# Performance work log

Measured on AMD Instinct MI355X. Metric: run time of the kernel, lower is better.

## Reference

```python
import jax, jax.numpy as jnp
import numpy as np

B, N, DIM = 2, 2048, 512
H, DH = 8, 64
INNER = H * DH
SCALE = DH ** -0.5


def setup_inputs() -> dict:
    key = jax.random.key(0)
    ks = jax.random.split(key, 8)
    s = 0.02
    return {
        "nodes": jax.random.normal(ks[0], (B, N, DIM), dtype=jnp.float32),
        "edge_mask": jax.random.bernoulli(ks[1], 0.9, (B, N, N)),
        "wq": jax.random.normal(ks[2], (DIM, INNER), dtype=jnp.float32) * s,
        "bq": jnp.zeros((INNER,), dtype=jnp.float32),
        "wkv": jax.random.normal(ks[3], (DIM, 2 * INNER), dtype=jnp.float32) * s,
        "bkv": jnp.zeros((2 * INNER,), dtype=jnp.float32),
        "wo": jax.random.normal(ks[4], (INNER, DIM), dtype=jnp.float32) * s,
        "bo": jnp.zeros((DIM,), dtype=jnp.float32),
    }


def reference(nodes, edge_mask, wq, bq, wkv, bkv, wo, bo):
    b, n, _ = nodes.shape
    q = nodes @ wq + bq                      # [b, n, h*dh]
    kv = nodes @ wkv + bkv                   # [b, n, 2*h*dh]
    k, v = jnp.split(kv, 2, axis=-1)
    # split heads -> [b, h, n, dh]
    split = lambda t: t.reshape(b, n, H, DH).transpose(0, 2, 1, 3)
    q, k, v = split(q), split(k), split(v)
    sim = jnp.einsum('bhid,bhjd->bhij', q, k) * SCALE
    max_neg = -jnp.finfo(sim.dtype).max
    sim = jnp.where(edge_mask[:, None, :, :], sim, max_neg)
    attn = jax.nn.softmax(sim, axis=-1)
    out = jnp.einsum('bhij,bhjd->bhid', attn, v)      # [b, h, n, dh]
    out = out.transpose(0, 2, 1, 3).reshape(b, n, INNER)
    return out @ wo + bo
```

## Files before the change

kernel.cpp:

```cpp
#include <hip/hip_runtime.h>
#include <cstdint>
#include <cstddef>

#define DEVI __device__ __forceinline__

typedef __bf16 bf16x8 __attribute__((ext_vector_type(8)));
typedef float floatx4 __attribute__((ext_vector_type(4)));
typedef unsigned short us4v __attribute__((ext_vector_type(4)));
typedef unsigned short us8 __attribute__((ext_vector_type(8)));

static_assert(sizeof(bf16x8) == 16, "bf16x8 must be 16B");
static_assert(sizeof(us8) == 16, "us8 must be 16B");


#if __has_builtin(__builtin_amdgcn_cvt_pk_bf16_f32)
DEVI unsigned short f2bf(float f) {
  typedef __bf16 bf16x2 __attribute__((ext_vector_type(2)));
  union { bf16x2 v; unsigned short u[2]; } c;
  c.v = __builtin_amdgcn_cvt_pk_bf16_f32(f, 0.f);
  return c.u[0];
}
#else
DEVI unsigned short f2bf(float f) {
  unsigned int u = __float_as_uint(f);
  u += 0x7fffu + ((u >> 16) & 1u);
  return (unsigned short)(u >> 16);
}
#endif

DEVI float exp2c(float x) {
#if __has_builtin(__builtin_amdgcn_exp2f)
  return __builtin_amdgcn_exp2f(x);
#else
  return exp2f(x);
#endif
}

DEVI bf16x8 ld8(const unsigned short* p) { return *(const bf16x8*)p; }

typedef const __attribute__((address_space(1))) void* gas_ptr;
typedef __attribute__((address_space(3))) void* las_ptr;

DEVI void gld16(const void* g, void* l) {
  __builtin_amdgcn_global_load_lds((gas_ptr)g, (las_ptr)l, 16, 0, 0);
}

#define WAIT_LGKM0() __builtin_amdgcn_s_waitcnt(0xc07f)


__global__ void detect_k(const unsigned int* m, int* flag) {
  __shared__ int bad;
  if (threadIdx.x == 0) bad = 0;
  __syncthreads();
  int loc = 0;
  for (int i = threadIdx.x; i < 4096; i += 256) {
    unsigned int v = m[i];
    if (v > 1u && v != 0x3f800000u) loc = 1;
  }
  if (loc) atomicOr(&bad, 1);
  __syncthreads();
  if (threadIdx.x == 0) *flag = bad;
}

__global__ __launch_bounds__(256) void pack_k(const void* m, const int* flag,
                                              unsigned int* pm) {
  int t = blockIdx.x * 256 + threadIdx.x;
  int lane = threadIdx.x & 63;
  int byteMode = *flag;
  unsigned int n;
  if (byteMode) {
    unsigned int x = ((const unsigned int*)m)[t];
    n = ((x & 0xffu) ? 1u : 0u) | ((x & 0xff00u) ? 2u : 0u) |
        ((x & 0xff0000u) ? 4u : 0u) | ((x >> 24) ? 8u : 0u);
  } else {
    uint4 v = ((const uint4*)m)[t];
    n = (v.x ? 1u : 0u) | (v.y ? 2u : 0u) | (v.z ? 4u : 0u) | (v.w ? 8u : 0u);
  }
  unsigned int w = n << ((lane & 7) * 4);
  w |= __shfl_xor(w, 1);
  w |= __shfl_xor(w, 2);
  w |= __shfl_xor(w, 4);
  if ((lane & 7) == 0) pm[t >> 3] = w;
}

__global__ void cvt_x_k(const float* __restrict__ x, unsigned short* __restrict__ xb) {
  int i = blockIdx.x * 256 + threadIdx.x;
  float4 v = ((const float4*)x)[i];
  us4v o;
  o[0] = f2bf(v.x); o[1] = f2bf(v.y); o[2] = f2bf(v.z); o[3] = f2bf(v.w);
  *(us4v*)(xb + (size_t)i * 4) = o;
}

__global__ __launch_bounds__(256) void transpose_w_k(const float* __restrict__ src,
                                                     unsigned short* __restrict__ dst,
                                                     int C, int c0) {
  __shared__ unsigned short t2[64 * 64];
  const int t = threadIdx.x;
  const int ct = blockIdx.x * 64, rt = blockIdx.y * 64;
  for (int p = 0; p < 4; p++) {
    int kl = p * 16 + (t >> 4);
    int cc = (t & 15) * 4;
    float4 v = *(const float4*)&src[(size_t)(rt + kl) * C + ct + cc];
    float f[4] = {v.x, v.y, v.z, v.w};
    for (int i = 0; i < 4; i++) {
      int c = cc + i;
      t2[c * 64 + (kl ^ (c & 56))] = f2bf(f[i]);
    }
  }
  __syncthreads();
  for (int p = 0; p < 2; p++) {
    int c = p * 32 + (t >> 3);
    int kc = (t & 7) * 8;
    us8 v = *(const us8*)&t2[c * 64 + (kc ^ (c & 56))];
    *(us8*)&dst[(size_t)(c0 + ct + c) * 512 + rt + kc] = v;
  }
}

__global__ __launch_bounds__(256) void transpose_v_k(const unsigned short* __restrict__ v,
                                                     unsigned short* __restrict__ vt) {
  __shared__ unsigned short t2[64 * 64];
  const int t = threadIdx.x;
  const int bh = blockIdx.y;
  const int nt = blockIdx.x * 64;
  const unsigned short* src = v + (size_t)bh * 2048 * 64;
  unsigned short* dst = vt + (size_t)bh * 64 * 2048;
  for (int p = 0; p < 2; p++) {
    int nl = p * 32 + (t >> 3);
    int dc = (t & 7) * 8;
    us8 in = *(const us8*)&src[(size_t)(nt + nl) * 64 + dc];
    for (int i = 0; i < 8; i++) {
      int d = dc + i;
      t2[d * 64 + (nl ^ (d & 56))] = in[i];
    }
  }
  __syncthreads();
  for (int p = 0; p < 2; p++) {
    int d = p * 32 + (t >> 3);
    int nc = (t & 7) * 8;
    us8 o = *(const us8*)&t2[d * 64 + (nc ^ (d & 56))];
    *(us8*)&dst[(size_t)d * 2048 + nt + nc] = o;
  }
}

__global__ __launch_bounds__(256) void gemm_qkv_k(
    const unsigned short* __restrict__ A,
    const unsigned short* __restrict__ Bt,
    const float* __restrict__ bq, const float* __restrict__ bkv,
    unsigned short* __restrict__ Qo, unsigned short* __restrict__ Ko,
    unsigned short* __restrict__ Vo) {
  __shared__ unsigned short smem[8192];
  unsigned short* sA = smem;
  unsigned short* sB = smem + 4096;
  const int tid = threadIdx.x;
  const int wave = tid >> 6, lane = tid & 63, quad = lane >> 4, l16 = lane & 15;
  const int wm = wave >> 1, wn = wave & 1;
  const int bm = blockIdx.x, bn = blockIdx.y;
  floatx4 acc[4][4] = {};
  const int srow = tid >> 2;
  const int sg = (tid & 3) ^ (srow & 3);
  for (int kt = 0; kt < 16; kt++) {
    __syncthreads();
    for (int p = 0; p < 2; p++) {
      int row = p * 64 + srow;
      int g = (tid & 3) ^ (row & 3);
      gld16(&A [(size_t)(bm * 128 + row) * 512 + kt * 32 + g * 8],
            &sA[(p * 256 + wave * 64) * 8]);
      gld16(&Bt[(size_t)(bn * 128 + row) * 512 + kt * 32 + g * 8],
            &sB[(p * 256 + wave * 64) * 8]);
    }
    __syncthreads();
    bf16x8 aF[4], bF[4];
    int swz = (quad ^ (l16 & 3)) * 8;
    for (int i = 0; i < 4; i++) aF[i] = ld8(&sA[(wm * 64 + i * 16 + l16) * 32 + swz]);
    for (int j = 0; j < 4; j++) bF[j] = ld8(&sB[(wn * 64 + j * 16 + l16) * 32 + swz]);
    for (int i = 0; i < 4; i++)
      for (int j = 0; j < 4; j++)
        acc[i][j] = __builtin_amdgcn_mfma_f32_16x16x32_bf16(aF[i], bF[j], acc[i][j], 0, 0, 0);
  }

  const int sec = bn * 2 + wn;
  float bias[4];
  float scale = 1.0f;
  if (sec < 8) {
    for (int j = 0; j < 4; j++) bias[j] = bq[sec * 64 + j * 16 + l16];
    scale = 0.18033688011112042f;
  } else {
    for (int j = 0; j < 4; j++) bias[j] = bkv[(sec - 8) * 64 + j * 16 + l16];
  }
  unsigned short* reg = smem + wave * 2048;
  for (int h = 0; h < 2; h++) {
    __syncthreads();
    for (int i2 = 0; i2 < 2; i2++) {
      int i = h * 2 + i2;
      for (int j = 0; j < 4; j++) {
        int csw = ((j ^ quad) * 16) + l16;
        for (int r = 0; r < 4; r++) {
          int rloc = i2 * 16 + quad * 4 + r;
          reg[rloc * 64 + csw] = f2bf((acc[i][j][r] + bias[j]) * scale);
        }
      }
    }
    __syncthreads();
    for (int p = 0; p < 4; p++) {
      int rloc = p * 8 + (lane >> 3);
      int c8 = lane & 7;
      int qr = (rloc >> 2) & 3;
      us8 v = *(const us8*)(reg + rloc * 64 + ((c8 * 8) ^ (qr * 16)));
      int gr = bm * 128 + wm * 64 + h * 32 + rloc;
      int n = gr & 2047, b = gr >> 11, d0 = c8 * 8;
      unsigned short* dst;
      if (sec < 8)       dst = Qo + ((size_t)(b * 8 + sec)      * 2048 + n) * 64 + d0;
      else if (sec < 16) dst = Ko + ((size_t)(b * 8 + sec - 8)  * 2048 + n) * 64 + d0;
      else               dst = Vo + ((size_t)(b * 8 + sec - 16) * 2048 + n) * 64 + d0;
      *(us8*)dst = v;
    }
  }
  (void)sg;
}

__global__ __launch_bounds__(256) void attn_k(
    const unsigned short* __restrict__ Q,
    const unsigned short* __restrict__ K,
    const unsigned short* __restrict__ Vt,
    const unsigned int* __restrict__ pm,
    unsigned short* __restrict__ AO) {
  __shared__ unsigned short kT[2][4096];
  __shared__ unsigned short vT[2][4096];
  __shared__ unsigned short pA[4][1024];
  const int tid = threadIdx.x;
  const int wave = tid >> 6, lane = tid & 63, quad = lane >> 4, l16 = lane & 15;
  const int qt = blockIdx.x, bh = blockIdx.y, b = bh >> 3, h = bh & 7;
  const int q0 = qt * 64 + wave * 16;
  const unsigned short* Qb = Q + (size_t)bh * 2048 * 64;
  const unsigned short* Kb = K + (size_t)bh * 2048 * 64;
  const unsigned short* Vb = Vt + (size_t)bh * 64 * 2048;
  const unsigned int* pmB = pm + (size_t)b * 2048 * 64;

  bf16x8 qF[2];
  qF[0] = ld8(&Qb[(size_t)(q0 + l16) * 64 + quad * 8]);
  qF[1] = ld8(&Qb[(size_t)(q0 + l16) * 64 + 32 + quad * 8]);

  floatx4 oacc[4] = {};
  float lrow[4] = {0.f, 0.f, 0.f, 0.f};

  const int srow = tid >> 3;
  const int sc = tid & 7;
  auto stageKV = [&](int tile, int buf) {
    const int k0 = tile * 64;
    for (int p = 0; p < 2; p++) {
      int row = p * 32 + srow;
      int g = sc ^ (row & 7);
      gld16(&Kb[(size_t)(k0 + row) * 64 + g * 8], &kT[buf][(p * 256 + wave * 64) * 8]);
      gld16(&Vb[(size_t)row * 2048 + k0 + g * 8], &vT[buf][(p * 256 + wave * 64) * 8]);
    }
  };

  stageKV(0, 0);
  const int sw0 = (quad ^ (l16 & 7)) * 8;
  const int sw1 = ((4 + quad) ^ (l16 & 7)) * 8;

  for (int it = 0; it < 32; ++it) {
    const int cur = it & 1;
    __syncthreads();
    if (it + 1 < 32) stageKV(it + 1, cur ^ 1);

    const unsigned short* kc = kT[cur];
    const unsigned short* vc = vT[cur];

    uint2 mw[4];
    for (int r = 0; r < 4; r++)
      mw[r] = *(const uint2*)&pmB[(size_t)(q0 + quad * 4 + r) * 64 + it * 2];

    floatx4 sim[4];
    for (int cb = 0; cb < 4; cb++) {
      bf16x8 kf0 = ld8(&kc[(cb * 16 + l16) * 64 + sw0]);
      bf16x8 kf1 = ld8(&kc[(cb * 16 + l16) * 64 + sw1]);
      floatx4 z = {0.f, 0.f, 0.f, 0.f};
      z = __builtin_amdgcn_mfma_f32_16x16x32_bf16(qF[0], kf0, z, 0, 0, 0);
      sim[cb] = __builtin_amdgcn_mfma_f32_16x16x32_bf16(qF[1], kf1, z, 0, 0, 0);
    }

    float pv[4][4];
    for (int r = 0; r < 4; r++) {
      unsigned int s0 = mw[r].x >> l16;
      unsigned int s1 = mw[r].y >> l16;
      float p0 = exp2c(sim[0][r]) * (float)(s0 & 1u);
      float p1 = exp2c(sim[1][r]) * (float)((s0 >> 16) & 1u);
      float p2 = exp2c(sim[2][r]) * (float)(s1 & 1u);
      float p3 = exp2c(sim[3][r]) * (float)((s1 >> 16) & 1u);
      lrow[r] += (p0 + p1) + (p2 + p3);
      pv[0][r] = p0; pv[1][r] = p1; pv[2][r] = p2; pv[3][r] = p3;
    }

    unsigned short* pw = pA[wave];
    const int ci = l16 & 7;
    for (int cb = 0; cb < 4; cb++) {
      int cg = cb * 2 + (l16 >> 3);
      for (int r = 0; r < 4; r++) {
        int row = quad * 4 + r;
        pw[row * 64 + ((cg ^ (row & 7)) * 8) + ci] = f2bf(pv[cb][r]);
      }
    }
    WAIT_LGKM0();
    bf16x8 pF0 = ld8(&pw[l16 * 64 + sw0]);
    bf16x8 pF1 = ld8(&pw[l16 * 64 + sw1]);
    for (int nb = 0; nb < 4; nb++) {
      bf16x8 vf0 = ld8(&vc[(nb * 16 + l16) * 64 + sw0]);
      bf16x8 vf1 = ld8(&vc[(nb * 16 + l16) * 64 + sw1]);
      oacc[nb] = __builtin_amdgcn_mfma_f32_16x16x32_bf16(pF0, vf0, oacc[nb], 0, 0, 0);
      oacc[nb] = __builtin_amdgcn_mfma_f32_16x16x32_bf16(pF1, vf1, oacc[nb], 0, 0, 0);
    }
  }

  for (int r = 0; r < 4; r++) {
    float s = lrow[r];
    s += __shfl_xor(s, 1, 16);
    s += __shfl_xor(s, 2, 16);
    s += __shfl_xor(s, 4, 16);
    s += __shfl_xor(s, 8, 16);
    lrow[r] = 1.0f / s;
  }

  unsigned short* pw = pA[wave];
  const int ci = l16 & 7;
  for (int nb = 0; nb < 4; nb++) {
    int cg = nb * 2 + (l16 >> 3);
    for (int r = 0; r < 4; r++) {
      int row = quad * 4 + r;
      pw[row * 64 + ((cg ^ (row & 7)) * 8) + ci] = f2bf(oacc[nb][r] * lrow[r]);
    }
  }
  WAIT_LGKM0();
  for (int p = 0; p < 2; p++) {
    int row = p * 8 + (lane >> 3);
    int c8 = lane & 7;
    us8 v = *(const us8*)&pw[row * 64 + ((c8 ^ (row & 7)) * 8)];
    *(us8*)&AO[((size_t)b * 2048 + q0 + row) * 512 + h * 64 + c8 * 8] = v;
  }
}

__global__ __launch_bounds__(256) void gemm_out_k(
    const unsigned short* __restrict__ A,
    const unsigned short* __restrict__ Bt,
    const float* __restrict__ bo, float* __restrict__ out) {
  __shared__ unsigned short sA[128 * 32];
  __shared__ unsigned short sB[128 * 32];
  const int tid = threadIdx.x;
  const int wave = tid >> 6, lane = tid & 63, quad = lane >> 4, l16 = lane & 15;
  const int wm = wave >> 1, wn = wave & 1;
  const int bm = blockIdx.x, bn = blockIdx.y;
  floatx4 acc[4][4] = {};
  const int srow = tid >> 2;
  for (int kt = 0; kt < 16; kt++) {
    __syncthreads();
    for (int p = 0; p < 2; p++) {
      int row = p * 64 + srow;
      int g = (tid & 3) ^ (row & 3);
      gld16(&A [(size_t)(bm * 128 + row) * 512 + kt * 32 + g * 8],
            &sA[(p * 256 + wave * 64) * 8]);
      gld16(&Bt[(size_t)(bn * 128 + row) * 512 + kt * 32 + g * 8],
            &sB[(p * 256 + wave * 64) * 8]);
    }
    __syncthreads();
    bf16x8 aF[4], bF[4];
    int swz = (quad ^ (l16 & 3)) * 8;
    for (int i = 0; i < 4; i++) aF[i] = ld8(&sA[(wm * 64 + i * 16 + l16) * 32 + swz]);
    for (int j = 0; j < 4; j++) bF[j] = ld8(&sB[(wn * 64 + j * 16 + l16) * 32 + swz]);
    for (int i = 0; i < 4; i++)
      for (int j = 0; j < 4; j++)
        acc[i][j] = __builtin_amdgcn_mfma_f32_16x16x32_bf16(aF[i], bF[j], acc[i][j], 0, 0, 0);
  }
  for (int i = 0; i < 4; i++) {
    for (int j = 0; j < 4; j++) {
      int gc = bn * 128 + wn * 64 + j * 16 + l16;
      for (int r = 0; r < 4; r++) {
        int gr = bm * 128 + wm * 64 + i * 16 + quad * 4 + r;
        out[(size_t)gr * 512 + gc] = acc[i][j][r] + bo[gc];
      }
    }
  }
}

extern "C" void kernel_launch(void* const* d_in, const int* in_sizes, int n_in,
                              void* d_out, int out_size, void* d_ws, size_t ws_size,
                              hipStream_t stream) {
  const float* nodes = (const float*)d_in[0];
  const void*  mask  = d_in[1];
  const float* wq    = (const float*)d_in[2];
  const float* bq    = (const float*)d_in[3];
  const float* wkv   = (const float*)d_in[4];
  const float* bkv   = (const float*)d_in[5];
  const float* wo    = (const float*)d_in[6];
  const float* bo    = (const float*)d_in[7];
  float* out = (float*)d_out;

  char* ws = (char*)d_ws;
  unsigned short* XB    = (unsigned short*)(ws + 0);
  unsigned short* WQKVT = (unsigned short*)(ws + 4194304);
  unsigned short* WOT   = (unsigned short*)(ws + 5767168);
  unsigned short* Qm    = (unsigned short*)(ws + 6291456);
  unsigned short* Km    = (unsigned short*)(ws + 10485760);
  unsigned short* Vm    = (unsigned short*)(ws + 14680064);
  unsigned short* VTm   = (unsigned short*)(ws + 18874368);
  unsigned short* AOm   = (unsigned short*)(ws + 23068672);
  unsigned int*   PM    = (unsigned int*)(ws + 27262976);
  int*            FLAG  = (int*)(ws + 28311552);

  detect_k<<<1, 256, 0, stream>>>((const unsigned int*)mask, FLAG);
  pack_k<<<8192, 256, 0, stream>>>(mask, FLAG, PM);
  cvt_x_k<<<2048, 256, 0, stream>>>(nodes, XB);
  transpose_w_k<<<dim3(8, 8),  256, 0, stream>>>(wq,  WQKVT, 512, 0);
  transpose_w_k<<<dim3(16, 8), 256, 0, stream>>>(wkv, WQKVT, 1024, 512);
  transpose_w_k<<<dim3(8, 8),  256, 0, stream>>>(wo,  WOT, 512, 0);
  gemm_qkv_k<<<dim3(32, 12), 256, 0, stream>>>(XB, WQKVT, bq, bkv, Qm, Km, Vm);
  transpose_v_k<<<dim3(32, 16), 256, 0, stream>>>(Vm, VTm);
  attn_k<<<dim3(32, 16), 256, 0, stream>>>(Qm, Km, VTm, PM, AOm);
  gemm_out_k<<<dim3(32, 4), 256, 0, stream>>>(AOm, WOT, bo, out);
}
```

Baseline: 184.8 us.

## Fuse launches, write V transposed from QKV GEMM, restructure attention kernel

```diff
diff --git a/kernel.cpp b/kernel.cpp
--- a/kernel.cpp
+++ b/kernel.cpp
@@ -8,6 +8,7 @@
 typedef float floatx4 __attribute__((ext_vector_type(4)));
 typedef unsigned short us4v __attribute__((ext_vector_type(4)));
 typedef unsigned short us8 __attribute__((ext_vector_type(8)));
+typedef short short4v __attribute__((ext_vector_type(4)));
 
 static_assert(sizeof(bf16x8) == 16, "bf16x8 must be 16B");
 static_assert(sizeof(us8) == 16, "us8 must be 16B");
@@ -47,29 +48,22 @@
 
 #define WAIT_LGKM0() __builtin_amdgcn_s_waitcnt(0xc07f)
 
-
-__global__ void detect_k(const unsigned int* m, int* flag) {
-  __shared__ int bad;
-  if (threadIdx.x == 0) bad = 0;
+__global__ __launch_bounds__(256) void pack_k(const void* m, unsigned int* pm) {
+  __shared__ int mode;
+  const unsigned int* md = (const unsigned int*)m;
+  unsigned int probe = md[threadIdx.x];
+  bool odd = (probe > 1u && probe != 0x3f800000u);
+  if (threadIdx.x == 0) mode = 0;
   __syncthreads();
-  int loc = 0;
-  for (int i = threadIdx.x; i < 4096; i += 256) {
-    unsigned int v = m[i];
-    if (v > 1u && v != 0x3f800000u) loc = 1;
-  }
-  if (loc) atomicOr(&bad, 1);
+  if (odd) atomicOr(&mode, 1);
   __syncthreads();
-  if (threadIdx.x == 0) *flag = bad;
-}
-
-__global__ __launch_bounds__(256) void pack_k(const void* m, const int* flag,
-                                              unsigned int* pm) {
+  int byteMode = mode;
+
   int t = blockIdx.x * 256 + threadIdx.x;
   int lane = threadIdx.x & 63;
-  int byteMode = *flag;
   unsigned int n;
   if (byteMode) {
-    unsigned int x = ((const unsigned int*)m)[t];
+    unsigned int x = md[t];
     n = ((x & 0xffu) ? 1u : 0u) | ((x & 0xff00u) ? 2u : 0u) |
         ((x & 0xff0000u) ? 4u : 0u) | ((x >> 24) ? 8u : 0u);
   } else {
@@ -91,9 +85,15 @@
   *(us4v*)(xb + (size_t)i * 4) = o;
 }
 
-__global__ __launch_bounds__(256) void transpose_w_k(const float* __restrict__ src,
-                                                     unsigned short* __restrict__ dst,
-                                                     int C, int c0) {
+__global__ __launch_bounds__(256) void transpose_all_k(
+    const float* __restrict__ wq, const float* __restrict__ wkv,
+    const float* __restrict__ wo,
+    unsigned short* __restrict__ WQKVT, unsigned short* __restrict__ WOT) {
+  const float* src; unsigned short* dst; int C, c0;
+  int z = blockIdx.z;
+  if (z == 0)      { if (blockIdx.x >= 8) return; src = wq;  dst = WQKVT; C = 512;  c0 = 0; }
+  else if (z == 1) { src = wkv; dst = WQKVT; C = 1024; c0 = 512; }
+  else             { if (blockIdx.x >= 8) return; src = wo;  dst = WOT;  C = 512;  c0 = 0; }
   __shared__ unsigned short t2[64 * 64];
   const int t = threadIdx.x;
   const int ct = blockIdx.x * 64, rt = blockIdx.y * 64;
@@ -116,64 +116,41 @@
   }
 }
 
-__global__ __launch_bounds__(256) void transpose_v_k(const unsigned short* __restrict__ v,
-                                                     unsigned short* __restrict__ vt) {
-  __shared__ unsigned short t2[64 * 64];
-  const int t = threadIdx.x;
-  const int bh = blockIdx.y;
-  const int nt = blockIdx.x * 64;
-  const unsigned short* src = v + (size_t)bh * 2048 * 64;
-  unsigned short* dst = vt + (size_t)bh * 64 * 2048;
-  for (int p = 0; p < 2; p++) {
-    int nl = p * 32 + (t >> 3);
-    int dc = (t & 7) * 8;
-    us8 in = *(const us8*)&src[(size_t)(nt + nl) * 64 + dc];
-    for (int i = 0; i < 8; i++) {
-      int d = dc + i;
-      t2[d * 64 + (nl ^ (d & 56))] = in[i];
-    }
-  }
-  __syncthreads();
-  for (int p = 0; p < 2; p++) {
-    int d = p * 32 + (t >> 3);
-    int nc = (t & 7) * 8;
-    us8 o = *(const us8*)&t2[d * 64 + (nc ^ (d & 56))];
-    *(us8*)&dst[(size_t)d * 2048 + nt + nc] = o;
-  }
-}
-
 __global__ __launch_bounds__(256) void gemm_qkv_k(
     const unsigned short* __restrict__ A,
     const unsigned short* __restrict__ Bt,
     const float* __restrict__ bq, const float* __restrict__ bkv,
     unsigned short* __restrict__ Qo, unsigned short* __restrict__ Ko,
-    unsigned short* __restrict__ Vo) {
+    unsigned short* __restrict__ VTo) {
   __shared__ unsigned short smem[8192];
   unsigned short* sA = smem;
-  unsigned short* sB = smem + 4096;
+  unsigned short* sB = smem + 2048;
   const int tid = threadIdx.x;
   const int wave = tid >> 6, lane = tid & 63, quad = lane >> 4, l16 = lane & 15;
   const int wm = wave >> 1, wn = wave & 1;
   const int bm = blockIdx.x, bn = blockIdx.y;
-  floatx4 acc[4][4] = {};
-  const int srow = tid >> 2;
-  const int sg = (tid & 3) ^ (srow & 3);
+  floatx4 acc[2][4] = {};
+  const int arow = lane >> 2;
+  const int ag = lane & 3;
   for (int kt = 0; kt < 16; kt++) {
     __syncthreads();
-    for (int p = 0; p < 2; p++) {
-      int row = p * 64 + srow;
-      int g = (tid & 3) ^ (row & 3);
-      gld16(&A [(size_t)(bm * 128 + row) * 512 + kt * 32 + g * 8],
-            &sA[(p * 256 + wave * 64) * 8]);
-      gld16(&Bt[(size_t)(bn * 128 + row) * 512 + kt * 32 + g * 8],
-            &sB[(p * 256 + wave * 64) * 8]);
-    }
-    __syncthreads();
-    bf16x8 aF[4], bF[4];
+    {
+      int rowA = wave * 16 + arow;
+      int gA = ag ^ (rowA & 3);
+      gld16(&A[(size_t)(bm * 64 + rowA) * 512 + kt * 32 + gA * 8], &sA[(wave * 16) * 32]);
+      for (int p = 0; p < 2; p++) {
+        int rowB = p * 64 + wave * 16 + arow;
+        int gB = ag ^ (rowB & 3);
+        gld16(&Bt[(size_t)(bn * 128 + rowB) * 512 + kt * 32 + gB * 8],
+              &sB[(p * 64 + wave * 16) * 32]);
+      }
+    }
+    __syncthreads();
+    bf16x8 aF[2], bF[4];
     int swz = (quad ^ (l16 & 3)) * 8;
-    for (int i = 0; i < 4; i++) aF[i] = ld8(&sA[(wm * 64 + i * 16 + l16) * 32 + swz]);
+    for (int i = 0; i < 2; i++) aF[i] = ld8(&sA[(wm * 32 + i * 16 + l16) * 32 + swz]);
     for (int j = 0; j < 4; j++) bF[j] = ld8(&sB[(wn * 64 + j * 16 + l16) * 32 + swz]);
-    for (int i = 0; i < 4; i++)
+    for (int i = 0; i < 2; i++)
       for (int j = 0; j < 4; j++)
         acc[i][j] = __builtin_amdgcn_mfma_f32_16x16x32_bf16(aF[i], bF[j], acc[i][j], 0, 0, 0);
   }
@@ -187,147 +164,142 @@
   } else {
     for (int j = 0; j < 4; j++) bias[j] = bkv[(sec - 8) * 64 + j * 16 + l16];
   }
-  unsigned short* reg = smem + wave * 2048;
-  for (int h = 0; h < 2; h++) {
-    __syncthreads();
-    for (int i2 = 0; i2 < 2; i2++) {
-      int i = h * 2 + i2;
+  const int gr0 = bm * 64 + wm * 32;
+  const int b = gr0 >> 11, n0 = gr0 & 2047;
+  unsigned short* pw = smem + wave * 2048;
+  __syncthreads();
+  if (sec < 16) {
+    for (int i = 0; i < 2; i++)
       for (int j = 0; j < 4; j++) {
-        int csw = ((j ^ quad) * 16) + l16;
+        int cg = j * 2 + (l16 >> 3), ci = l16 & 7;
         for (int r = 0; r < 4; r++) {
-          int rloc = i2 * 16 + quad * 4 + r;
-          reg[rloc * 64 + csw] = f2bf((acc[i][j][r] + bias[j]) * scale);
+          int row = i * 16 + quad * 4 + r;
+          pw[row * 64 + ((cg ^ (row & 7)) * 8) + ci] = f2bf((acc[i][j][r] + bias[j]) * scale);
         }
       }
-    }
-    __syncthreads();
+    WAIT_LGKM0();
+    unsigned short* dst = (sec < 8) ? Qo + ((size_t)(b * 8 + sec) * 2048 + n0) * 64
+                                    : Ko + ((size_t)(b * 8 + sec - 8) * 2048 + n0) * 64;
     for (int p = 0; p < 4; p++) {
-      int rloc = p * 8 + (lane >> 3);
+      int row = p * 8 + (lane >> 3);
       int c8 = lane & 7;
-      int qr = (rloc >> 2) & 3;
-      us8 v = *(const us8*)(reg + rloc * 64 + ((c8 * 8) ^ (qr * 16)));
-      int gr = bm * 128 + wm * 64 + h * 32 + rloc;
-      int n = gr & 2047, b = gr >> 11, d0 = c8 * 8;
-      unsigned short* dst;
-      if (sec < 8)       dst = Qo + ((size_t)(b * 8 + sec)      * 2048 + n) * 64 + d0;
-      else if (sec < 16) dst = Ko + ((size_t)(b * 8 + sec - 8)  * 2048 + n) * 64 + d0;
-      else               dst = Vo + ((size_t)(b * 8 + sec - 16) * 2048 + n) * 64 + d0;
-      *(us8*)dst = v;
-    }
-  }
-  (void)sg;
-}
-
-__global__ __launch_bounds__(256) void attn_k(
+      us8 v = *(const us8*)&pw[row * 64 + ((c8 ^ (row & 7)) * 8)];
+      *(us8*)&dst[(size_t)row * 64 + c8 * 8] = v;
+    }
+  } else {
+    for (int i = 0; i < 2; i++)
+      for (int j = 0; j < 4; j++) {
+        int d = j * 16 + l16;
+        int ng = i * 2 + (quad >> 1), n7 = (quad & 1) * 4;
+        for (int r = 0; r < 4; r++)
+          pw[d * 32 + ((ng ^ (d & 3)) * 8) + n7 + r] = f2bf(acc[i][j][r] + bias[j]);
+      }
+    WAIT_LGKM0();
+    unsigned short* dst = VTo + (size_t)(b * 8 + sec - 16) * 64 * 2048 + n0;
+    for (int p = 0; p < 4; p++) {
+      int d = p * 16 + (lane >> 2);
+      int c4 = lane & 3;
+      us8 v = *(const us8*)&pw[d * 32 + ((c4 ^ (d & 3)) * 8)];
+      *(us8*)&dst[(size_t)d * 2048 + c4 * 8] = v;
+    }
+  }
+}
+
+__global__ __launch_bounds__(128, 4) void attn_k(
     const unsigned short* __restrict__ Q,
     const unsigned short* __restrict__ K,
     const unsigned short* __restrict__ Vt,
     const unsigned int* __restrict__ pm,
     unsigned short* __restrict__ AO) {
-  __shared__ unsigned short kT[2][4096];
-  __shared__ unsigned short vT[2][4096];
-  __shared__ unsigned short pA[4][1024];
+  __shared__ unsigned short kT[4096];
+  __shared__ unsigned short vT[4096];
+  __shared__ unsigned short pA[2][1024];
   const int tid = threadIdx.x;
   const int wave = tid >> 6, lane = tid & 63, quad = lane >> 4, l16 = lane & 15;
   const int qt = blockIdx.x, bh = blockIdx.y, b = bh >> 3, h = bh & 7;
-  const int q0 = qt * 64 + wave * 16;
+  const int q0 = qt * 32 + wave * 16;
   const unsigned short* Qb = Q + (size_t)bh * 2048 * 64;
   const unsigned short* Kb = K + (size_t)bh * 2048 * 64;
   const unsigned short* Vb = Vt + (size_t)bh * 64 * 2048;
   const unsigned int* pmB = pm + (size_t)b * 2048 * 64;
 
-  bf16x8 qF[2];
-  qF[0] = ld8(&Qb[(size_t)(q0 + l16) * 64 + quad * 8]);
-  qF[1] = ld8(&Qb[(size_t)(q0 + l16) * 64 + 32 + quad * 8]);
+  bf16x8 qF0 = ld8(&Qb[(size_t)(q0 + l16) * 64 + quad * 8]);
+  bf16x8 qF1 = ld8(&Qb[(size_t)(q0 + l16) * 64 + 32 + quad * 8]);
 
   floatx4 oacc[4] = {};
-  float lrow[4] = {0.f, 0.f, 0.f, 0.f};
-
-  const int srow = tid >> 3;
-  const int sc = tid & 7;
-  auto stageKV = [&](int tile, int buf) {
-    const int k0 = tile * 64;
-    for (int p = 0; p < 2; p++) {
-      int row = p * 32 + srow;
-      int g = sc ^ (row & 7);
-      gld16(&Kb[(size_t)(k0 + row) * 64 + g * 8], &kT[buf][(p * 256 + wave * 64) * 8]);
-      gld16(&Vb[(size_t)row * 2048 + k0 + g * 8], &vT[buf][(p * 256 + wave * 64) * 8]);
-    }
-  };
-
-  stageKV(0, 0);
+  float lsum = 0.f;
+
   const int sw0 = (quad ^ (l16 & 7)) * 8;
   const int sw1 = ((4 + quad) ^ (l16 & 7)) * 8;
+  const int srow = wave * 8 + (lane >> 3);
+  const int sg = lane & 7;
+  const int vg = ((quad >> 1) ^ (l16 & 7)) * 8;
 
   for (int it = 0; it < 32; ++it) {
-    const int cur = it & 1;
-    __syncthreads();
-    if (it + 1 < 32) stageKV(it + 1, cur ^ 1);
-
-    const unsigned short* kc = kT[cur];
-    const unsigned short* vc = vT[cur];
-
-    uint2 mw[4];
-    for (int r = 0; r < 4; r++)
-      mw[r] = *(const uint2*)&pmB[(size_t)(q0 + quad * 4 + r) * 64 + it * 2];
-
-    floatx4 sim[4];
-    for (int cb = 0; cb < 4; cb++) {
-      bf16x8 kf0 = ld8(&kc[(cb * 16 + l16) * 64 + sw0]);
-      bf16x8 kf1 = ld8(&kc[(cb * 16 + l16) * 64 + sw1]);
+    const int k0 = it * 64;
+    __syncthreads();
+    for (int p = 0; p < 4; p++) {
+      int row = p * 16 + srow;
+      int g = sg ^ (row & 7);
+      gld16(&Kb[(size_t)(k0 + row) * 64 + g * 8], &kT[(p * 16 + wave * 8) * 64]);
+      gld16(&Vb[(size_t)row * 2048 + k0 + g * 8], &vT[(p * 16 + wave * 8) * 64]);
+    }
+    uint2 mw = *(const uint2*)&pmB[(size_t)(q0 + l16) * 64 + it * 2];
+    __syncthreads();
+
+    floatx4 st[4];
+    for (int kb = 0; kb < 4; kb++) {
+      bf16x8 kf0 = ld8(&kT[(kb * 16 + l16) * 64 + sw0]);
+      bf16x8 kf1 = ld8(&kT[(kb * 16 + l16) * 64 + sw1]);
       floatx4 z = {0.f, 0.f, 0.f, 0.f};
-      z = __builtin_amdgcn_mfma_f32_16x16x32_bf16(qF[0], kf0, z, 0, 0, 0);
-      sim[cb] = __builtin_amdgcn_mfma_f32_16x16x32_bf16(qF[1], kf1, z, 0, 0, 0);
-    }
-
-    float pv[4][4];
+      z = __builtin_amdgcn_mfma_f32_16x16x32_bf16(kf0, qF0, z, 0, 0, 0);
+      st[kb] = __builtin_amdgcn_mfma_f32_16x16x32_bf16(kf1, qF1, z, 0, 0, 0);
+    }
+
+    union { short4v s4; unsigned short u[4]; unsigned int d[2]; } pf[4];
+    for (int kb = 0; kb < 4; kb++) {
+      unsigned int w = (kb < 2) ? mw.x : mw.y;
+      int base = (kb & 1) * 16 + quad * 4;
+      for (int r = 0; r < 4; r++) {
+        float e = exp2c(st[kb][r]);
+        e = ((w >> (base + r)) & 1u) ? e : 0.f;
+        lsum += e;
+        pf[kb].u[r] = f2bf(e);
+      }
+    }
+
+#if __has_builtin(__builtin_amdgcn_mfma_f32_16x16x16bf16_1k)
+    for (int kb = 0; kb < 4; kb++) {
+      int off = ((kb * 2 + (quad >> 1)) ^ (l16 & 7)) * 8 + (quad & 1) * 4;
+      for (int db = 0; db < 4; db++) {
+        short4v a = *(const short4v*)&vT[(db * 16 + l16) * 64 + off];
+        oacc[db] = __builtin_amdgcn_mfma_f32_16x16x16bf16_1k(a, pf[kb].s4, oacc[db], 0, 0, 0);
+      }
+    }
+#else
+    for (int kb = 0; kb < 4; kb++) {
+      union { bf16x8 v; unsigned int d[4]; } bf;
+      if (quad & 1) { bf.d[0] = 0; bf.d[1] = 0; bf.d[2] = pf[kb].d[0]; bf.d[3] = pf[kb].d[1]; }
+      else          { bf.d[0] = pf[kb].d[0]; bf.d[1] = pf[kb].d[1]; bf.d[2] = 0; bf.d[3] = 0; }
+      int off = ((kb * 2 + (quad >> 1)) ^ (l16 & 7)) * 8;
+      for (int db = 0; db < 4; db++) {
+        bf16x8 a = ld8(&vT[(db * 16 + l16) * 64 + off]);
+        oacc[db] = __builtin_amdgcn_mfma_f32_16x16x32_bf16(a, bf.v, oacc[db], 0, 0, 0);
+      }
+    }
+#endif
+  }
+
+  lsum += __shfl_xor(lsum, 16);
+  lsum += __shfl_xor(lsum, 32);
+  float inv = 1.0f / lsum;
+
+  unsigned short* pw = pA[wave];
+  for (int db = 0; db < 4; db++) {
+    int cg = db * 2 + (quad >> 1);
     for (int r = 0; r < 4; r++) {
-      unsigned int s0 = mw[r].x >> l16;
-      unsigned int s1 = mw[r].y >> l16;
-      float p0 = exp2c(sim[0][r]) * (float)(s0 & 1u);
-      float p1 = exp2c(sim[1][r]) * (float)((s0 >> 16) & 1u);
-      float p2 = exp2c(sim[2][r]) * (float)(s1 & 1u);
-      float p3 = exp2c(sim[3][r]) * (float)((s1 >> 16) & 1u);
-      lrow[r] += (p0 + p1) + (p2 + p3);
-      pv[0][r] = p0; pv[1][r] = p1; pv[2][r] = p2; pv[3][r] = p3;
-    }
-
-    unsigned short* pw = pA[wave];
-    const int ci = l16 & 7;
-    for (int cb = 0; cb < 4; cb++) {
-      int cg = cb * 2 + (l16 >> 3);
-      for (int r = 0; r < 4; r++) {
-        int row = quad * 4 + r;
-        pw[row * 64 + ((cg ^ (row & 7)) * 8) + ci] = f2bf(pv[cb][r]);
-      }
-    }
-    WAIT_LGKM0();
-    bf16x8 pF0 = ld8(&pw[l16 * 64 + sw0]);
-    bf16x8 pF1 = ld8(&pw[l16 * 64 + sw1]);
-    for (int nb = 0; nb < 4; nb++) {
-      bf16x8 vf0 = ld8(&vc[(nb * 16 + l16) * 64 + sw0]);
-      bf16x8 vf1 = ld8(&vc[(nb * 16 + l16) * 64 + sw1]);
-      oacc[nb] = __builtin_amdgcn_mfma_f32_16x16x32_bf16(pF0, vf0, oacc[nb], 0, 0, 0);
-      oacc[nb] = __builtin_amdgcn_mfma_f32_16x16x32_bf16(pF1, vf1, oacc[nb], 0, 0, 0);
-    }
-  }
-
-  for (int r = 0; r < 4; r++) {
-    float s = lrow[r];
-    s += __shfl_xor(s, 1, 16);
-    s += __shfl_xor(s, 2, 16);
-    s += __shfl_xor(s, 4, 16);
-    s += __shfl_xor(s, 8, 16);
-    lrow[r] = 1.0f / s;
-  }
-
-  unsigned short* pw = pA[wave];
-  const int ci = l16 & 7;
-  for (int nb = 0; nb < 4; nb++) {
-    int cg = nb * 2 + (l16 >> 3);
-    for (int r = 0; r < 4; r++) {
-      int row = quad * 4 + r;
-      pw[row * 64 + ((cg ^ (row & 7)) * 8) + ci] = f2bf(oacc[nb][r] * lrow[r]);
+      int col = db * 16 + quad * 4 + r;
+      pw[l16 * 64 + ((cg ^ (l16 & 7)) * 8) + (col & 7)] = f2bf(oacc[db][r] * inv);
     }
   }
   WAIT_LGKM0();
@@ -337,48 +309,54 @@
     us8 v = *(const us8*)&pw[row * 64 + ((c8 ^ (row & 7)) * 8)];
     *(us8*)&AO[((size_t)b * 2048 + q0 + row) * 512 + h * 64 + c8 * 8] = v;
   }
+  (void)vg;
 }
 
 __global__ __launch_bounds__(256) void gemm_out_k(
     const unsigned short* __restrict__ A,
     const unsigned short* __restrict__ Bt,
     const float* __restrict__ bo, float* __restrict__ out) {
-  __shared__ unsigned short sA[128 * 32];
-  __shared__ unsigned short sB[128 * 32];
+  __shared__ unsigned short smem[6144];
+  unsigned short* sA = smem;
+  unsigned short* sB = smem + 2048;
   const int tid = threadIdx.x;
   const int wave = tid >> 6, lane = tid & 63, quad = lane >> 4, l16 = lane & 15;
   const int wm = wave >> 1, wn = wave & 1;
   const int bm = blockIdx.x, bn = blockIdx.y;
-  floatx4 acc[4][4] = {};
-  const int srow = tid >> 2;
+  floatx4 acc[2][4] = {};
+  const int arow = lane >> 2;
+  const int ag = lane & 3;
   for (int kt = 0; kt < 16; kt++) {
     __syncthreads();
-    for (int p = 0; p < 2; p++) {
-      int row = p * 64 + srow;
-      int g = (tid & 3) ^ (row & 3);
-      gld16(&A [(size_t)(bm * 128 + row) * 512 + kt * 32 + g * 8],
-            &sA[(p * 256 + wave * 64) * 8]);
-      gld16(&Bt[(size_t)(bn * 128 + row) * 512 + kt * 32 + g * 8],
-            &sB[(p * 256 + wave * 64) * 8]);
-    }
-    __syncthreads();
-    bf16x8 aF[4], bF[4];
+    {
+      int rowA = wave * 16 + arow;
+      int gA = ag ^ (rowA & 3);
+      gld16(&A[(size_t)(bm * 64 + rowA) * 512 + kt * 32 + gA * 8], &sA[(wave * 16) * 32]);
+      for (int p = 0; p < 2; p++) {
+        int rowB = p * 64 + wave * 16 + arow;
+        int gB = ag ^ (rowB & 3);
+        gld16(&Bt[(size_t)(bn * 128 + rowB) * 512 + kt * 32 + gB * 8],
+              &sB[(p * 64 + wave * 16) * 32]);
+      }
+    }
+    __syncthreads();
+    bf16x8 aF[2], bF[4];
     int swz = (quad ^ (l16 & 3)) * 8;
-    for (int i = 0; i < 4; i++) aF[i] = ld8(&sA[(wm * 64 + i * 16 + l16) * 32 + swz]);
+    for (int i = 0; i < 2; i++) aF[i] = ld8(&sA[(wm * 32 + i * 16 + l16) * 32 + swz]);
     for (int j = 0; j < 4; j++) bF[j] = ld8(&sB[(wn * 64 + j * 16 + l16) * 32 + swz]);
-    for (int i = 0; i < 4; i++)
+    for (int i = 0; i < 2; i++)
       for (int j = 0; j < 4; j++)
         acc[i][j] = __builtin_amdgcn_mfma_f32_16x16x32_bf16(aF[i], bF[j], acc[i][j], 0, 0, 0);
   }
-  for (int i = 0; i < 4; i++) {
+  for (int i = 0; i < 2; i++)
     for (int j = 0; j < 4; j++) {
       int gc = bn * 128 + wn * 64 + j * 16 + l16;
+      float bb = bo[gc];
       for (int r = 0; r < 4; r++) {
-        int gr = bm * 128 + wm * 64 + i * 16 + quad * 4 + r;
-        out[(size_t)gr * 512 + gc] = acc[i][j][r] + bo[gc];
-      }
-    }
-  }
+        int gr = bm * 64 + wm * 32 + i * 16 + quad * 4 + r;
+        out[(size_t)gr * 512 + gc] = acc[i][j][r] + bb;
+      }
+    }
 }
 
 extern "C" void kernel_launch(void* const* d_in, const int* in_sizes, int n_in,
@@ -400,20 +378,14 @@
   unsigned short* WOT   = (unsigned short*)(ws + 5767168);
   unsigned short* Qm    = (unsigned short*)(ws + 6291456);
   unsigned short* Km    = (unsigned short*)(ws + 10485760);
-  unsigned short* Vm    = (unsigned short*)(ws + 14680064);
   unsigned short* VTm   = (unsigned short*)(ws + 18874368);
   unsigned short* AOm   = (unsigned short*)(ws + 23068672);
   unsigned int*   PM    = (unsigned int*)(ws + 27262976);
-  int*            FLAG  = (int*)(ws + 28311552);
-
-  detect_k<<<1, 256, 0, stream>>>((const unsigned int*)mask, FLAG);
-  pack_k<<<8192, 256, 0, stream>>>(mask, FLAG, PM);
+
+  pack_k<<<8192, 256, 0, stream>>>(mask, PM);
   cvt_x_k<<<2048, 256, 0, stream>>>(nodes, XB);
-  transpose_w_k<<<dim3(8, 8),  256, 0, stream>>>(wq,  WQKVT, 512, 0);
-  transpose_w_k<<<dim3(16, 8), 256, 0, stream>>>(wkv, WQKVT, 1024, 512);
-  transpose_w_k<<<dim3(8, 8),  256, 0, stream>>>(wo,  WOT, 512, 0);
-  gemm_qkv_k<<<dim3(32, 12), 256, 0, stream>>>(XB, WQKVT, bq, bkv, Qm, Km, Vm);
-  transpose_v_k<<<dim3(32, 16), 256, 0, stream>>>(Vm, VTm);
-  attn_k<<<dim3(32, 16), 256, 0, stream>>>(Qm, Km, VTm, PM, AOm);
-  gemm_out_k<<<dim3(32, 4), 256, 0, stream>>>(AOm, WOT, bo, out);
-}
+  transpose_all_k<<<dim3(16, 8, 3), 256, 0, stream>>>(wq, wkv, wo, WQKVT, WOT);
+  gemm_qkv_k<<<dim3(64, 12), 256, 0, stream>>>(XB, WQKVT, bq, bkv, Qm, Km, VTm);
+  attn_k<<<dim3(64, 16), 128, 0, stream>>>(Qm, Km, VTm, PM, AOm);
+  gemm_out_k<<<dim3(64, 4), 256, 0, stream>>>(AOm, WOT, bo, out);
+}
```

Result: faster. 169.6 us (-8.2%).
